# Optimization experiments

Hardware: AMD Instinct MI355X
Metric: run time of the kernel (lower is better)

The kernel has to match this reference:

```python
import jax, jax.numpy as jnp
import numpy as np


def _tri(x):
    # triangle wave, period=0.1, amplitude=1:
    # (a/p) * (p - |x % (2p) - p| - p/2) = 10 * (0.05 - |x % 0.2 - 0.1|)
    return 10.0 * (0.05 - jnp.abs(jnp.mod(x, 0.2) - 0.1))


def _cdist(a, b):
    # pairwise Euclidean distance between rows of a [n, d] and b [m, d]
    d2 = jnp.sum((a[:, None, :] - b[None, :, :]) ** 2, axis=-1)
    return jnp.sqrt(jnp.maximum(d2, 0.0))


def setup_inputs() -> dict:
    key = jax.random.key(0)
    ks = jax.random.split(key, 8)
    B, L, D = 131072, 256, 20
    x = jax.random.normal(ks[0], (B, L), dtype=jnp.float32)
    # layer_params ~ U(-1, 1) of shape [l, dimensions]
    p0, p1, p2, p3 = (jax.random.uniform(ks[1 + i], (L, D), dtype=jnp.float32,
                                         minval=-1.0, maxval=1.0) for i in range(4))
    # layer_biases ~ U(-0.1, 0.1) of shape [l, 1]; bias[0] is never used in forward
    b1, b2, b3 = (jax.random.uniform(ks[5 + i], (L, 1), dtype=jnp.float32,
                                     minval=-0.1, maxval=0.1) for i in range(3))
    return {"x": x, "p0": p0, "p1": p1, "p2": p2, "p3": p3,
            "b1": b1, "b2": b2, "b3": b3}


def reference(x, p0, p1, p2, p3, b1, b2, b3):
    params = [p0, p1, p2, p3]
    biases = [None, b1, b2, b3]  # forward only uses biases[i+1]
    n = len(params)
    z = x
    for i in range(n - 1):
        scale = 1.0 / np.sqrt(params[i].shape[0]).astype(np.float32)
        W = _tri(_cdist(params[i], params[i + 1])) * scale  # [l_i, l_{i+1}]
        z = z @ W + biases[i + 1].T                          # [B, l_{i+1}]
        if i < n - 2:
            z = jax.nn.relu(z)
    return z
```

## Files before the change

### kernel.cpp

```cpp
#include <hip/hip_runtime.h>
#include <hip/hip_bf16.h>
#include <hip/hip_fp16.h>

typedef _Float16 half8 __attribute__((ext_vector_type(8)));
typedef _Float16 half4 __attribute__((ext_vector_type(4)));
typedef float    floatx4 __attribute__((ext_vector_type(4)));

#define BM 64

__global__ void make_weights_frag(const float* __restrict__ p0, const float* __restrict__ p1,
                                  const float* __restrict__ p2, const float* __restrict__ p3,
                                  _Float16* __restrict__ wt) {
    int idx  = blockIdx.x * blockDim.x + threadIdx.x;
    int lane = idx & 63;
    int nf   = (idx >> 6) & 3;
    int s    = (idx >> 8) & 7;
    int wc   = (idx >> 11) & 3;
    int l    = idx >> 13;
    int n  = wc * 64 + nf * 16 + (lane & 15);
    int k0 = s * 32 + (lane >> 4) * 8;
    const float* P[4] = {p0, p1, p2, p3};
    const float* pb = P[l + 1] + n * 20;
    float pbr[20];
    #pragma unroll
    for (int i = 0; i < 20; ++i) pbr[i] = pb[i];
    half8 o;
    #pragma unroll
    for (int j = 0; j < 8; ++j) {
        const float* pa = P[l] + (k0 + j) * 20;
        float d2 = 0.f;
        #pragma unroll
        for (int i = 0; i < 20; ++i) { float df = pa[i] - pbr[i]; d2 += df * df; }
        float d = sqrtf(d2);
        float m = fmodf(d, 0.2f);
        o[j] = (_Float16)(10.0f * (0.05f - fabsf(m - 0.1f)) * 0.0625f);
    }
    *reinterpret_cast<half8*>(wt + (size_t)idx * 8) = o;
}

__global__ __launch_bounds__(512, 4) void pcn_fused(
    const float* __restrict__ x, const _Float16* __restrict__ wt,
    const float* __restrict__ b1, const float* __restrict__ b2,
    const float* __restrict__ b3, float* __restrict__ out) {

    __shared__ __align__(16) _Float16 zlds[BM * 256];

    const int t    = threadIdx.x;
    const int lane = t & 63;
    const int wid  = t >> 6;
    const int wr   = wid >> 2;
    const int wc   = wid & 3;
    const int l15  = lane & 15;
    const int lg   = lane >> 4;
    const size_t row0 = (size_t)blockIdx.x * BM;

    char* zb = reinterpret_cast<char*>(zlds);

    const _Float16* wl = wt + ((size_t)wc << 14);

    half8 bb[2][4];
    #pragma unroll
    for (int nf = 0; nf < 4; ++nf)
        bb[0][nf] = *reinterpret_cast<const half8*>(wl + nf * 512 + lane * 8);

    {
        floatx4 xr[8];
        #pragma unroll
        for (int i = 0; i < 8; ++i) {
            int g   = i * 512 + t;
            int row = g >> 6, c4 = g & 63;
            xr[i] = *reinterpret_cast<const floatx4*>(x + (row0 + row) * 256 + c4 * 4);
        }
        #pragma unroll
        for (int i = 0; i < 8; ++i) {
            int g   = i * 512 + t;
            int row = g >> 6, c4 = g & 63;
            half4 h;
            h[0] = (_Float16)xr[i][0]; h[1] = (_Float16)xr[i][1];
            h[2] = (_Float16)xr[i][2]; h[3] = (_Float16)xr[i][3];
            int chunk = (c4 >> 1) ^ (row & 7);
            *reinterpret_cast<half4*>(zb + row * 512 + chunk * 16 + (c4 & 1) * 8) = h;
        }
    }
    __syncthreads();

    floatx4 acc[2][4];

    for (int l = 0; l < 3; ++l) {
        const float* bias = (l == 0) ? b1 : (l == 1) ? b2 : b3;

        #pragma unroll
        for (int nf = 0; nf < 4; ++nf) {
            const float bv = bias[wc * 64 + nf * 16 + l15];
            #pragma unroll
            for (int mf = 0; mf < 2; ++mf)
                acc[mf][nf] = floatx4{bv, bv, bv, bv};
        }

        #pragma unroll
        for (int s = 0; s < 8; ++s) {
            if (s < 7) {
                #pragma unroll
                for (int nf = 0; nf < 4; ++nf)
                    bb[(s + 1) & 1][nf] = *reinterpret_cast<const half8*>(
                        wl + (s + 1) * 2048 + nf * 512 + lane * 8);
            }
            const int vchunk = (s * 4 + lg) ^ (l15 & 7);
            half8 a[2];
            #pragma unroll
            for (int mf = 0; mf < 2; ++mf)
                a[mf] = *reinterpret_cast<const half8*>(
                    zb + (wr * 32 + mf * 16 + l15) * 512 + vchunk * 16);
            #pragma unroll
            for (int mf = 0; mf < 2; ++mf)
                #pragma unroll
                for (int nf = 0; nf < 4; ++nf)
                    acc[mf][nf] = __builtin_amdgcn_mfma_f32_16x16x32_f16(
                        a[mf], bb[s & 1][nf], acc[mf][nf], 0, 0, 0);
        }

        if (l < 2) {
            wl += (size_t)4 << 14;
            #pragma unroll
            for (int nf = 0; nf < 4; ++nf)
                bb[0][nf] = *reinterpret_cast<const half8*>(wl + nf * 512 + lane * 8);
        }

        __syncthreads();

        if (l < 2) {
            #pragma unroll
            for (int nf = 0; nf < 4; ++nf) {
                const int n = wc * 64 + nf * 16 + l15;
                #pragma unroll
                for (int mf = 0; mf < 2; ++mf) {
                    const int mrow = wr * 32 + mf * 16 + lg * 4;
                    #pragma unroll
                    for (int r = 0; r < 4; ++r) {
                        float v = fmaxf(acc[mf][nf][r], 0.0f);
                        const int row  = mrow + r;
                        const int byte = row * 512 + (((n >> 3) ^ (row & 7)) << 4)
                                       + (n & 7) * 2;
                        *reinterpret_cast<_Float16*>(zb + byte) = (_Float16)v;
                    }
                }
            }
            __syncthreads();
        } else {
            #pragma unroll
            for (int nf = 0; nf < 4; ++nf) {
                const int n = wc * 64 + nf * 16 + l15;
                #pragma unroll
                for (int mf = 0; mf < 2; ++mf) {
                    const size_t mrow = row0 + wr * 32 + mf * 16 + lg * 4;
                    #pragma unroll
                    for (int r = 0; r < 4; ++r)
                        out[(mrow + r) * 256 + n] = acc[mf][nf][r];
                }
            }
        }
    }
}

extern "C" void kernel_launch(void* const* d_in, const int* in_sizes, int n_in,
                              void* d_out, int out_size, void* d_ws, size_t ws_size,
                              hipStream_t stream) {
    const float* x  = (const float*)d_in[0];
    const float* p0 = (const float*)d_in[1];
    const float* p1 = (const float*)d_in[2];
    const float* p2 = (const float*)d_in[3];
    const float* p3 = (const float*)d_in[4];
    const float* b1 = (const float*)d_in[5];
    const float* b2 = (const float*)d_in[6];
    const float* b3 = (const float*)d_in[7];
    float* out = (float*)d_out;
    _Float16* wt = (_Float16*)d_ws;

    const int B = in_sizes[0] / 256;

    make_weights_frag<<<96, 256, 0, stream>>>(p0, p1, p2, p3, wt);
    pcn_fused<<<B / BM, 512, 0, stream>>>(x, wt, b1, b2, b3, out);
}
```

Measured before the change: 97.64 us.

## Double-buffer activation LDS and prefetch weight fragments two steps ahead across layers

Splits the activation tile into two LDS buffers that alternate between layers, which removes the barrier that used to sit between the last read of one layer and the writeback of the next. Weight fragment loads move to a three-slot ring indexed globally across all 24 k-steps, so prefetch now crosses layer boundaries, and the layer loop is fully unrolled. The cost is LDS per block growing from 32KB to 64KB, which may cut resident blocks per CU, plus extra registers for the third fragment slot.

```diff
diff --git a/kernel.cpp b/kernel.cpp
--- a/kernel.cpp
+++ b/kernel.cpp
@@ -43,7 +43,7 @@
     const float* __restrict__ b1, const float* __restrict__ b2,
     const float* __restrict__ b3, float* __restrict__ out) {
 
-    __shared__ __align__(16) _Float16 zlds[BM * 256];
+    __shared__ __align__(16) _Float16 zlds[2][BM * 256];
 
     const int t    = threadIdx.x;
     const int lane = t & 63;
@@ -54,14 +54,17 @@
     const int lg   = lane >> 4;
     const size_t row0 = (size_t)blockIdx.x * BM;
 
-    char* zb = reinterpret_cast<char*>(zlds);
+    char* const zb0 = reinterpret_cast<char*>(&zlds[0][0]);
+    char* const zb1 = reinterpret_cast<char*>(&zlds[1][0]);
 
-    const _Float16* wl = wt + ((size_t)wc << 14);
+    half8   bb[3][4];
+    floatx4 acc[2][4];
 
-    half8 bb[2][4];
-    #pragma unroll
-    for (int nf = 0; nf < 4; ++nf)
-        bb[0][nf] = *reinterpret_cast<const half8*>(wl + nf * 512 + lane * 8);
+    auto wfrag = [&](int g, int nf) -> const half8* {
+        const int gl = g >> 3, gs = g & 7;
+        return reinterpret_cast<const half8*>(
+            wt + (((size_t)gl * 4 + wc) << 14) + gs * 2048 + nf * 512 + lane * 8);
+    };
 
     {
         floatx4 xr[8];
@@ -79,15 +82,19 @@
             h[0] = (_Float16)xr[i][0]; h[1] = (_Float16)xr[i][1];
             h[2] = (_Float16)xr[i][2]; h[3] = (_Float16)xr[i][3];
             int chunk = (c4 >> 1) ^ (row & 7);
-            *reinterpret_cast<half4*>(zb + row * 512 + chunk * 16 + (c4 & 1) * 8) = h;
+            *reinterpret_cast<half4*>(zb0 + row * 512 + chunk * 16 + (c4 & 1) * 8) = h;
         }
     }
+    #pragma unroll
+    for (int nf = 0; nf < 4; ++nf) bb[0][nf] = *wfrag(0, nf);
+    #pragma unroll
+    for (int nf = 0; nf < 4; ++nf) bb[1][nf] = *wfrag(1, nf);
     __syncthreads();
 
-    floatx4 acc[2][4];
-
+    #pragma unroll
     for (int l = 0; l < 3; ++l) {
         const float* bias = (l == 0) ? b1 : (l == 1) ? b2 : b3;
+        char* const rz = (l == 1) ? zb1 : zb0;
 
         #pragma unroll
         for (int nf = 0; nf < 4; ++nf) {
@@ -99,36 +106,28 @@
 
         #pragma unroll
         for (int s = 0; s < 8; ++s) {
-            if (s < 7) {
+            const int g = l * 8 + s;
+            if (g + 2 < 24) {
                 #pragma unroll
                 for (int nf = 0; nf < 4; ++nf)
-                    bb[(s + 1) & 1][nf] = *reinterpret_cast<const half8*>(
-                        wl + (s + 1) * 2048 + nf * 512 + lane * 8);
+                    bb[(g + 2) % 3][nf] = *wfrag(g + 2, nf);
             }
             const int vchunk = (s * 4 + lg) ^ (l15 & 7);
             half8 a[2];
             #pragma unroll
             for (int mf = 0; mf < 2; ++mf)
                 a[mf] = *reinterpret_cast<const half8*>(
-                    zb + (wr * 32 + mf * 16 + l15) * 512 + vchunk * 16);
+                    rz + (wr * 32 + mf * 16 + l15) * 512 + vchunk * 16);
             #pragma unroll
             for (int mf = 0; mf < 2; ++mf)
                 #pragma unroll
                 for (int nf = 0; nf < 4; ++nf)
                     acc[mf][nf] = __builtin_amdgcn_mfma_f32_16x16x32_f16(
-                        a[mf], bb[s & 1][nf], acc[mf][nf], 0, 0, 0);
+                        a[mf], bb[g % 3][nf], acc[mf][nf], 0, 0, 0);
         }
 
         if (l < 2) {
-            wl += (size_t)4 << 14;
-            #pragma unroll
-            for (int nf = 0; nf < 4; ++nf)
-                bb[0][nf] = *reinterpret_cast<const half8*>(wl + nf * 512 + lane * 8);
-        }
-
-        __syncthreads();
-
-        if (l < 2) {
+            char* const wz = (l == 0) ? zb1 : zb0;
             #pragma unroll
             for (int nf = 0; nf < 4; ++nf) {
                 const int n = wc * 64 + nf * 16 + l15;
@@ -141,7 +140,7 @@
                         const int row  = mrow + r;
                         const int byte = row * 512 + (((n >> 3) ^ (row & 7)) << 4)
                                        + (n & 7) * 2;
-                        *reinterpret_cast<_Float16*>(zb + byte) = (_Float16)v;
+                        *reinterpret_cast<_Float16*>(wz + byte) = (_Float16)v;
                     }
                 }
             }
```

Result: no change. 95.82 us (-1.9%).

## Use 4 waves per block, each computing all 64 rows for its column slice

Applied to the files above, without the earlier changes.

The fused MLP kernel drops from 8 waves (2 row groups by 4 column groups) to 4 waves per block. Each wave now covers all 64 rows of the block tile for its 64 output columns, so every weight fragment loaded from global memory feeds 16 MFMAs instead of 8. This halves weight-load traffic per row and removes the block-wide barrier before the final store. In exchange, the doubled accumulator tile raises register pressure and there are fewer waves per block to hide latency. The layer loop is also fully unrolled and the x tile is loaded in four batches.

```diff
diff --git a/kernel.cpp b/kernel.cpp
--- a/kernel.cpp
+++ b/kernel.cpp
@@ -38,7 +38,7 @@
     *reinterpret_cast<half8*>(wt + (size_t)idx * 8) = o;
 }
 
-__global__ __launch_bounds__(512, 4) void pcn_fused(
+__global__ __launch_bounds__(256, 4) void pcn_fused(
     const float* __restrict__ x, const _Float16* __restrict__ wt,
     const float* __restrict__ b1, const float* __restrict__ b2,
     const float* __restrict__ b3, float* __restrict__ out) {
@@ -47,33 +47,28 @@
 
     const int t    = threadIdx.x;
     const int lane = t & 63;
-    const int wid  = t >> 6;
-    const int wr   = wid >> 2;
-    const int wc   = wid & 3;
+    const int wc   = t >> 6;
     const int l15  = lane & 15;
     const int lg   = lane >> 4;
     const size_t row0 = (size_t)blockIdx.x * BM;
 
-    char* zb = reinterpret_cast<char*>(zlds);
+    char* const zb = reinterpret_cast<char*>(zlds);
 
-    const _Float16* wl = wt + ((size_t)wc << 14);
+    half8   bb[2][4];
+    floatx4 acc[4][4];
 
-    half8 bb[2][4];
     #pragma unroll
-    for (int nf = 0; nf < 4; ++nf)
-        bb[0][nf] = *reinterpret_cast<const half8*>(wl + nf * 512 + lane * 8);
-
-    {
-        floatx4 xr[8];
+    for (int b = 0; b < 4; ++b) {
+        floatx4 xr[4];
         #pragma unroll
-        for (int i = 0; i < 8; ++i) {
-            int g   = i * 512 + t;
+        for (int i = 0; i < 4; ++i) {
+            int g   = (b * 4 + i) * 256 + t;
             int row = g >> 6, c4 = g & 63;
             xr[i] = *reinterpret_cast<const floatx4*>(x + (row0 + row) * 256 + c4 * 4);
         }
         #pragma unroll
-        for (int i = 0; i < 8; ++i) {
-            int g   = i * 512 + t;
+        for (int i = 0; i < 4; ++i) {
+            int g   = (b * 4 + i) * 256 + t;
             int row = g >> 6, c4 = g & 63;
             half4 h;
             h[0] = (_Float16)xr[i][0]; h[1] = (_Float16)xr[i][1];
@@ -82,18 +77,24 @@
             *reinterpret_cast<half4*>(zb + row * 512 + chunk * 16 + (c4 & 1) * 8) = h;
         }
     }
+    {
+        const _Float16* w0 = wt + ((size_t)wc << 14);
+        #pragma unroll
+        for (int nf = 0; nf < 4; ++nf)
+            bb[0][nf] = *reinterpret_cast<const half8*>(w0 + nf * 512 + lane * 8);
+    }
     __syncthreads();
 
-    floatx4 acc[2][4];
-
+    #pragma unroll
     for (int l = 0; l < 3; ++l) {
         const float* bias = (l == 0) ? b1 : (l == 1) ? b2 : b3;
+        const _Float16* wlp = wt + (((size_t)l * 4 + wc) << 14);
 
         #pragma unroll
         for (int nf = 0; nf < 4; ++nf) {
             const float bv = bias[wc * 64 + nf * 16 + l15];
             #pragma unroll
-            for (int mf = 0; mf < 2; ++mf)
+            for (int mf = 0; mf < 4; ++mf)
                 acc[mf][nf] = floatx4{bv, bv, bv, bv};
         }
 
@@ -103,16 +104,16 @@
                 #pragma unroll
                 for (int nf = 0; nf < 4; ++nf)
                     bb[(s + 1) & 1][nf] = *reinterpret_cast<const half8*>(
-                        wl + (s + 1) * 2048 + nf * 512 + lane * 8);
+                        wlp + (s + 1) * 2048 + nf * 512 + lane * 8);
             }
             const int vchunk = (s * 4 + lg) ^ (l15 & 7);
-            half8 a[2];
+            half8 a[4];
             #pragma unroll
-            for (int mf = 0; mf < 2; ++mf)
+            for (int mf = 0; mf < 4; ++mf)
                 a[mf] = *reinterpret_cast<const half8*>(
-                    zb + (wr * 32 + mf * 16 + l15) * 512 + vchunk * 16);
+                    zb + (mf * 16 + l15) * 512 + vchunk * 16);
             #pragma unroll
-            for (int mf = 0; mf < 2; ++mf)
+            for (int mf = 0; mf < 4; ++mf)
                 #pragma unroll
                 for (int nf = 0; nf < 4; ++nf)
                     acc[mf][nf] = __builtin_amdgcn_mfma_f32_16x16x32_f16(
@@ -120,21 +121,20 @@
         }
 
         if (l < 2) {
-            wl += (size_t)4 << 14;
+            const _Float16* wn = wt + (((size_t)(l + 1) * 4 + wc) << 14);
             #pragma unroll
             for (int nf = 0; nf < 4; ++nf)
-                bb[0][nf] = *reinterpret_cast<const half8*>(wl + nf * 512 + lane * 8);
+                bb[0][nf] = *reinterpret_cast<const half8*>(wn + nf * 512 + lane * 8);
         }
 
-        __syncthreads();
-
         if (l < 2) {
+            __syncthreads();
             #pragma unroll
             for (int nf = 0; nf < 4; ++nf) {
                 const int n = wc * 64 + nf * 16 + l15;
                 #pragma unroll
-                for (int mf = 0; mf < 2; ++mf) {
-                    const int mrow = wr * 32 + mf * 16 + lg * 4;
+                for (int mf = 0; mf < 4; ++mf) {
+                    const int mrow = mf * 16 + lg * 4;
                     #pragma unroll
                     for (int r = 0; r < 4; ++r) {
                         float v = fmaxf(acc[mf][nf][r], 0.0f);
@@ -151,8 +151,8 @@
             for (int nf = 0; nf < 4; ++nf) {
                 const int n = wc * 64 + nf * 16 + l15;
                 #pragma unroll
-                for (int mf = 0; mf < 2; ++mf) {
-                    const size_t mrow = row0 + wr * 32 + mf * 16 + lg * 4;
+                for (int mf = 0; mf < 4; ++mf) {
+                    const size_t mrow = row0 + mf * 16 + lg * 4;
                     #pragma unroll
                     for (int r = 0; r < 4; ++r)
                         out[(mrow + r) * 256 + n] = acc[mf][nf][r];
@@ -179,5 +179,5 @@
     const int B = in_sizes[0] / 256;
 
     make_weights_frag<<<96, 256, 0, stream>>>(p0, p1, p2, p3, wt);
-    pcn_fused<<<B / BM, 512, 0, stream>>>(x, wt, b1, b2, b3, out);
+    pcn_fused<<<B / BM, 256, 0, stream>>>(x, wt, b1, b2, b3, out);
 }
```

Result: slower. 146.8 us (+50.3%).
